# Performance work log

Hardware: AMD Instinct MI355X
Metric: run time of the kernel (lower is better)

## Reference

```python
import jax, jax.numpy as jnp
import numpy as np

N = 10000   # num_nodes (= input feature dim, identity-style features)
E = 320000  # edges (avg degree 32)
P = 200000  # candidate node pairs
H1, H2 = 32, 16


def gcn_conv(x, W, b, edge_index, num_nodes):
    # PyG GCNConv: add self-loops, symmetric D^-1/2 (A+I) D^-1/2 normalization,
    # linear transform, scatter-add aggregation, then bias.
    loop = jnp.arange(num_nodes)
    src = jnp.concatenate([edge_index[0], loop])
    dst = jnp.concatenate([edge_index[1], loop])
    deg = jax.ops.segment_sum(jnp.ones_like(src, dtype=x.dtype), dst,
                              num_segments=num_nodes)  # includes self-loop, so deg >= 1
    dinv = jax.lax.rsqrt(deg)
    norm = dinv[src] * dinv[dst]                       # [E+N]
    h = x @ W                                          # [N, out]
    out = jax.ops.segment_sum(h[src] * norm[:, None], dst, num_segments=num_nodes)
    return out + b


def setup_inputs() -> dict:
    key = jax.random.key(0)
    ks = jax.random.split(key, 9)
    x = jax.random.normal(ks[0], (N, N), dtype=jnp.float32)
    edge_index = jax.random.randint(ks[1], (2, E), 0, N)
    pair_index = jax.random.randint(ks[2], (P, 2), 0, N)
    W1 = jax.random.normal(ks[3], (N, H1), dtype=jnp.float32) * 0.01
    b1 = jnp.zeros((H1,), jnp.float32)
    W2 = jax.random.normal(ks[4], (H1, H2), dtype=jnp.float32) * 0.1
    b2 = jnp.zeros((H2,), jnp.float32)
    Wfc = jax.random.normal(ks[5], (2 * H2, 1), dtype=jnp.float32) * 0.1
    bfc = jnp.zeros((1,), jnp.float32)
    return {"x": x, "edge_index": edge_index, "pair_index": pair_index,
            "W1": W1, "b1": b1, "W2": W2, "b2": b2, "Wfc": Wfc, "bfc": bfc}


def reference(x, edge_index, pair_index, W1, b1, W2, b2, Wfc, bfc):
    h = jax.nn.relu(gcn_conv(x, W1, b1, edge_index, N))   # [N, 32]
    h = gcn_conv(h, W2, b2, edge_index, N)                # [N, 16]
    pair = jnp.concatenate([h[pair_index[:, 0]], h[pair_index[:, 1]]], axis=1)  # [P, 32]
    return jax.nn.sigmoid(pair @ Wfc + bfc)               # [P, 1]
```

## Files before the change

### kernel.cpp

```cpp
#include <hip/hip_runtime.h>
#include <math.h>

#define NN 10000
#define EE 320000
#define PP 200000
#define WKP 10240

typedef __attribute__((ext_vector_type(8))) short bf8v;
typedef __attribute__((ext_vector_type(4))) float f4v;

#define GLOAD_LDS16(gsrc, ldst)                                                        \
    __builtin_amdgcn_global_load_lds((const __attribute__((address_space(1))) void*)(gsrc), \
                                     (__attribute__((address_space(3))) void*)(ldst), 16, 0, 0)

__device__ __forceinline__ ushort f2bf(float f) {
    uint u = __float_as_uint(f);
    return (ushort)((u + 0x7fffu + ((u >> 16) & 1u)) >> 16);
}

__global__ void k_deg_count(const int* __restrict__ dst, int* __restrict__ degi) {
    int e = blockIdx.x * blockDim.x + threadIdx.x;
    if (e < EE) atomicAdd(&degi[dst[e]], 1);
}

__global__ void k_dinv(const int* __restrict__ degi, float* __restrict__ dinv) {
    int n = blockIdx.x * blockDim.x + threadIdx.x;
    if (n < NN) dinv[n] = rsqrtf((float)(degi[n] + 1));
}

__global__ void k_wprep(const float* __restrict__ W1, ushort* __restrict__ w1t) {
    int t = blockIdx.x * blockDim.x + threadIdx.x;
    if (t >= 32 * WKP) return;
    int c = t / WKP, k = t - c * WKP;
    float v = (k < NN) ? W1[(long)k * 32 + c] : 0.f;
    w1t[t] = f2bf(v);
}

__global__ __launch_bounds__(256) void k_gemm1(const float* __restrict__ x,
                                               const ushort* __restrict__ w1t,
                                               const float* __restrict__ zp,
                                               float* __restrict__ h1_pre) {
    __shared__ __align__(16) float xs[4][3][32][32];
    const int tid = threadIdx.x;
    const int lane = tid & 63;
    const int w = tid >> 6;
    const int lr = lane >> 3;
    const int s = lane & 7;
    const int fl = lane & 15;
    const int khi = lane >> 4;
    const int row0 = blockIdx.x * 128 + w * 32;
    const int k_begin = blockIdx.y * 640;
    const int k_end = min(NN, k_begin + 640);
    const int nt = (k_end - k_begin + 31) >> 5;
    const long NN2 = (long)NN * NN;

    f4v acc[2][2];
#pragma unroll
    for (int a = 0; a < 2; ++a)
#pragma unroll
        for (int b = 0; b < 2; ++b) acc[a][b] = (f4v){0.f, 0.f, 0.f, 0.f};

    auto stage_x = [&](int buf, int t) {
        const int k0 = k_begin + t * 32;
#pragma unroll
        for (int j = 0; j < 4; ++j) {
            int rl = j * 8 + lr;
            int c4 = s ^ (rl & 7);
            long flat = (long)(row0 + rl) * NN + k0 + c4 * 4;
            const float* src = (flat + 4 <= NN2) ? (x + flat) : zp;
            GLOAD_LDS16(src, &xs[w][buf][j * 8][0]);
        }
    };
    auto wload = [&](int t, bf8v& b0, bf8v& b1) {
        const long kg = (long)k_begin + t * 32 + khi * 8;
        b0 = *(const bf8v*)(w1t + (long)(fl)      * WKP + kg);
        b1 = *(const bf8v*)(w1t + (long)(16 + fl) * WKP + kg);
    };
    auto compute = [&](int buf, bf8v b0, bf8v b1) {
#pragma unroll
        for (int rt = 0; rt < 2; ++rt) {
            const int rowl = rt * 16 + fl;
            const float4* xr = (const float4*)&xs[w][buf][rowl][0];
            float4 f0 = xr[(khi * 2)     ^ (rowl & 7)];
            float4 f1 = xr[(khi * 2 + 1) ^ (rowl & 7)];
            union { bf8v v; ushort u[8]; } a;
            a.u[0] = f2bf(f0.x); a.u[1] = f2bf(f0.y); a.u[2] = f2bf(f0.z); a.u[3] = f2bf(f0.w);
            a.u[4] = f2bf(f1.x); a.u[5] = f2bf(f1.y); a.u[6] = f2bf(f1.z); a.u[7] = f2bf(f1.w);
            acc[rt][0] = __builtin_amdgcn_mfma_f32_16x16x32_bf16(a.v, b0, acc[rt][0], 0, 0, 0);
            acc[rt][1] = __builtin_amdgcn_mfma_f32_16x16x32_bf16(a.v, b1, acc[rt][1], 0, 0, 0);
        }
    };

    bf8v wc0, wc1, wn0, wn1;
    stage_x(0, 0);
    stage_x(1, 1);
    wload(0, wc0, wc1);

    int buf = 0;
    for (int t = 0; t < nt; ++t) {
        if (t + 2 < nt) stage_x((buf + 2 == 3 ? buf - 1 : buf + 2), t + 2);
        if (t + 1 < nt) wload(t + 1, wn0, wn1);
        asm volatile("s_waitcnt vmcnt(6)" ::: "memory");
        __builtin_amdgcn_sched_barrier(0);
        compute(buf, wc0, wc1);
        wc0 = wn0; wc1 = wn1;
        buf = (buf + 1 == 3) ? 0 : buf + 1;
    }

#pragma unroll
    for (int rt = 0; rt < 2; ++rt) {
        const int gbase = row0 + rt * 16 + khi * 4;
#pragma unroll
        for (int ct = 0; ct < 2; ++ct) {
            const int col = ct * 16 + fl;
#pragma unroll
            for (int r = 0; r < 4; ++r) {
                const int g = gbase + r;
                if (g < NN) atomicAdd(&h1_pre[g * 32 + col], acc[rt][ct][r]);
            }
        }
    }
}

__global__ void k_selfinit1(const float* __restrict__ h1_pre, const float* __restrict__ dinv,
                            float* __restrict__ out1) {
    int t = blockIdx.x * blockDim.x + threadIdx.x;
    if (t < NN * 32) {
        int n = t >> 5;
        float di = dinv[n];
        out1[t] = di * di * h1_pre[t];
    }
}

__global__ void k_scatter1(const int* __restrict__ src, const int* __restrict__ dst,
                           const float* __restrict__ dinv, const float* __restrict__ h1_pre,
                           float* __restrict__ out1) {
    int t = blockIdx.x * blockDim.x + threadIdx.x;
    if (t >= EE * 32) return;
    int e = t >> 5, c = t & 31;
    int s = src[e], d = dst[e];
    float nrm = dinv[s] * dinv[d];
    atomicAdd(&out1[d * 32 + c], h1_pre[s * 32 + c] * nrm);
}

__global__ void k_bias_relu1(float* __restrict__ out1, const float* __restrict__ b1) {
    int t = blockIdx.x * blockDim.x + threadIdx.x;
    if (t < NN * 32) out1[t] = fmaxf(out1[t] + b1[t & 31], 0.f);
}

__global__ __launch_bounds__(256) void k_gemm2(const float* __restrict__ out1,
                                               const float* __restrict__ W2,
                                               float* __restrict__ h2_pre) {
    __shared__ float w2s[512];
    int tid = threadIdx.x;
    w2s[tid] = W2[tid & 511];
    if (tid < 256) w2s[256 + tid] = W2[256 + tid];
    __syncthreads();
    int c = tid & 15, yloc = tid >> 4;
    int n = blockIdx.x * 16 + yloc;
    if (n < NN) {
        float a = 0.f;
#pragma unroll
        for (int k = 0; k < 32; ++k) a += out1[n * 32 + k] * w2s[k * 16 + c];
        h2_pre[n * 16 + c] = a;
    }
}

__global__ void k_selfinit2(const float* __restrict__ h2_pre, const float* __restrict__ dinv,
                            float* __restrict__ out2) {
    int t = blockIdx.x * blockDim.x + threadIdx.x;
    if (t < NN * 16) {
        int n = t >> 4;
        float di = dinv[n];
        out2[t] = di * di * h2_pre[t];
    }
}

__global__ void k_scatter2(const int* __restrict__ src, const int* __restrict__ dst,
                           const float* __restrict__ dinv, const float* __restrict__ h2_pre,
                           float* __restrict__ out2) {
    int t = blockIdx.x * blockDim.x + threadIdx.x;
    if (t >= EE * 16) return;
    int e = t >> 4, c = t & 15;
    int s = src[e], d = dst[e];
    float nrm = dinv[s] * dinv[d];
    atomicAdd(&out2[d * 16 + c], h2_pre[s * 16 + c] * nrm);
}

__global__ void k_final2(const float* __restrict__ out2, const float* __restrict__ b2,
                         const float* __restrict__ Wfc, float* __restrict__ s_arr,
                         float* __restrict__ t_arr) {
    int n = blockIdx.x * blockDim.x + threadIdx.x;
    if (n >= NN) return;
    float s = 0.f, t = 0.f;
#pragma unroll
    for (int c = 0; c < 16; ++c) {
        float v = out2[n * 16 + c] + b2[c];
        s += v * Wfc[c];
        t += v * Wfc[16 + c];
    }
    s_arr[n] = s;
    t_arr[n] = t;
}

__global__ void k_pairs(const int* __restrict__ pair, const float* __restrict__ s_arr,
                        const float* __restrict__ t_arr, const float* __restrict__ bfc,
                        float* __restrict__ out) {
    int p = blockIdx.x * blockDim.x + threadIdx.x;
    if (p >= PP) return;
    const int2 ab = ((const int2*)pair)[p];
    float z = s_arr[ab.x] + t_arr[ab.y] + bfc[0];
    out[p] = 1.f / (1.f + expf(-z));
}

extern "C" void kernel_launch(void* const* d_in, const int* in_sizes, int n_in,
                              void* d_out, int out_size, void* d_ws, size_t ws_size,
                              hipStream_t stream) {
    const float* x    = (const float*)d_in[0];
    const int*   edge = (const int*)d_in[1];
    const int*   pair = (const int*)d_in[2];
    const float* W1   = (const float*)d_in[3];
    const float* b1   = (const float*)d_in[4];
    const float* W2   = (const float*)d_in[5];
    const float* b2   = (const float*)d_in[6];
    const float* Wfc  = (const float*)d_in[7];
    const float* bfc  = (const float*)d_in[8];
    float* out = (float*)d_out;
    float* ws  = (float*)d_ws;

    const int* src = edge;
    const int* dst = edge + EE;

    int*    degi   = (int*)ws;
    float*  dinv   = ws + NN;
    float*  h1_pre = ws + 2 * NN;
    float*  out1   = ws + 34 * NN;
    float*  h2_pre = ws + 66 * NN;
    float*  out2   = ws + 82 * NN;
    float*  s_arr  = ws + 98 * NN;
    float*  t_arr  = ws + 99 * NN;
    float*  zp     = ws + 100 * NN;
    ushort* w1t    = (ushort*)(ws + 100 * NN + 256);

    hipMemsetAsync(degi, 0, NN * sizeof(int), stream);
    hipMemsetAsync(h1_pre, 0, NN * 32 * sizeof(float), stream);
    hipMemsetAsync(zp, 0, 1024, stream);

    k_deg_count<<<(EE + 255) / 256, 256, 0, stream>>>(dst, degi);
    k_dinv<<<(NN + 255) / 256, 256, 0, stream>>>(degi, dinv);
    k_wprep<<<(32 * WKP + 255) / 256, 256, 0, stream>>>(W1, w1t);

    k_gemm1<<<dim3(79, 16), 256, 0, stream>>>(x, w1t, zp, h1_pre);

    k_selfinit1<<<(NN * 32 + 255) / 256, 256, 0, stream>>>(h1_pre, dinv, out1);
    k_scatter1<<<(EE * 32 + 255) / 256, 256, 0, stream>>>(src, dst, dinv, h1_pre, out1);
    k_bias_relu1<<<(NN * 32 + 255) / 256, 256, 0, stream>>>(out1, b1);

    k_gemm2<<<(NN + 15) / 16, 256, 0, stream>>>(out1, W2, h2_pre);

    k_selfinit2<<<(NN * 16 + 255) / 256, 256, 0, stream>>>(h2_pre, dinv, out2);
    k_scatter2<<<(EE * 16 + 255) / 256, 256, 0, stream>>>(src, dst, dinv, h2_pre, out2);

    k_final2<<<(NN + 255) / 256, 256, 0, stream>>>(out2, b2, Wfc, s_arr, t_arr);
    k_pairs<<<(PP + 255) / 256, 256, 0, stream>>>(pair, s_arr, t_arr, bfc, out);
}
```

Before: 207.3 us.

## Pre-swizzle W1 into MFMA fragment order and stage via LDS double buffer

W1 is now prepared in per-tile MFMA fragment layout so each wave loads its B operand with contiguous 16-byte global-to-LDS loads alongside the x tile. The x pipeline drops from triple to double buffering, and the register-held prefetch of W is replaced by LDS reads. This is meant to coalesce the B loads and simplify the wait accounting. In exchange it gives up one stage of prefetch depth, which may expose more of the load latency of the memory-bound x stream.

Result: faster. 198.9 us (-4.1%).

```diff
diff --git a/kernel.cpp b/kernel.cpp
--- a/kernel.cpp
+++ b/kernel.cpp
@@ -4,7 +4,7 @@
 #define NN 10000
 #define EE 320000
 #define PP 200000
-#define WKP 10240
+#define NTILES 320
 
 typedef __attribute__((ext_vector_type(8))) short bf8v;
 typedef __attribute__((ext_vector_type(4))) float f4v;
@@ -28,19 +28,21 @@
     if (n < NN) dinv[n] = rsqrtf((float)(degi[n] + 1));
 }
 
-__global__ void k_wprep(const float* __restrict__ W1, ushort* __restrict__ w1t) {
-    int t = blockIdx.x * blockDim.x + threadIdx.x;
-    if (t >= 32 * WKP) return;
-    int c = t / WKP, k = t - c * WKP;
-    float v = (k < NN) ? W1[(long)k * 32 + c] : 0.f;
-    w1t[t] = f2bf(v);
+__global__ void k_wprep(const float* __restrict__ W1, ushort* __restrict__ wf) {
+    int t = blockIdx.x * blockDim.x + threadIdx.x;
+    if (t >= NTILES * 2 * 64 * 8) return;
+    int e = t & 7, lane = (t >> 3) & 63, ct = (t >> 9) & 1, g = t >> 10;
+    int col = ct * 16 + (lane & 15);
+    int k = g * 32 + (lane >> 4) * 8 + e;
+    wf[t] = (k < NN) ? f2bf(W1[(long)k * 32 + col]) : (ushort)0;
 }
 
 __global__ __launch_bounds__(256) void k_gemm1(const float* __restrict__ x,
-                                               const ushort* __restrict__ w1t,
+                                               const ushort* __restrict__ wf,
                                                const float* __restrict__ zp,
                                                float* __restrict__ h1_pre) {
-    __shared__ __align__(16) float xs[4][3][32][32];
+    __shared__ __align__(16) float  xs[4][2][32][32];
+    __shared__ __align__(16) ushort ws[4][2][1024];
     const int tid = threadIdx.x;
     const int lane = tid & 63;
     const int w = tid >> 6;
@@ -51,6 +53,7 @@
     const int row0 = blockIdx.x * 128 + w * 32;
     const int k_begin = blockIdx.y * 640;
     const int k_end = min(NN, k_begin + 640);
+    const int g0 = blockIdx.y * 20;
     const int nt = (k_end - k_begin + 31) >> 5;
     const long NN2 = (long)NN * NN;
 
@@ -60,7 +63,7 @@
 #pragma unroll
         for (int b = 0; b < 2; ++b) acc[a][b] = (f4v){0.f, 0.f, 0.f, 0.f};
 
-    auto stage_x = [&](int buf, int t) {
+    auto stage = [&](int buf, int t) {
         const int k0 = k_begin + t * 32;
 #pragma unroll
         for (int j = 0; j < 4; ++j) {
@@ -70,13 +73,14 @@
             const float* src = (flat + 4 <= NN2) ? (x + flat) : zp;
             GLOAD_LDS16(src, &xs[w][buf][j * 8][0]);
         }
+        const int g = g0 + t;
+#pragma unroll
+        for (int ct = 0; ct < 2; ++ct)
+            GLOAD_LDS16(wf + ((long)(g * 2 + ct) * 64 + lane) * 8, &ws[w][buf][ct * 512]);
     };
-    auto wload = [&](int t, bf8v& b0, bf8v& b1) {
-        const long kg = (long)k_begin + t * 32 + khi * 8;
-        b0 = *(const bf8v*)(w1t + (long)(fl)      * WKP + kg);
-        b1 = *(const bf8v*)(w1t + (long)(16 + fl) * WKP + kg);
-    };
-    auto compute = [&](int buf, bf8v b0, bf8v b1) {
+    auto compute = [&](int buf) {
+        bf8v b0 = *(const bf8v*)&ws[w][buf][lane * 8];
+        bf8v b1 = *(const bf8v*)&ws[w][buf][512 + lane * 8];
 #pragma unroll
         for (int rt = 0; rt < 2; ++rt) {
             const int rowl = rt * 16 + fl;
@@ -91,20 +95,18 @@
         }
     };
 
-    bf8v wc0, wc1, wn0, wn1;
-    stage_x(0, 0);
-    stage_x(1, 1);
-    wload(0, wc0, wc1);
-
+    stage(0, 0);
     int buf = 0;
     for (int t = 0; t < nt; ++t) {
-        if (t + 2 < nt) stage_x((buf + 2 == 3 ? buf - 1 : buf + 2), t + 2);
-        if (t + 1 < nt) wload(t + 1, wn0, wn1);
-        asm volatile("s_waitcnt vmcnt(6)" ::: "memory");
+        if (t + 1 < nt) {
+            stage(buf ^ 1, t + 1);
+            asm volatile("s_waitcnt vmcnt(6)" ::: "memory");
+        } else {
+            asm volatile("s_waitcnt vmcnt(0)" ::: "memory");
+        }
         __builtin_amdgcn_sched_barrier(0);
-        compute(buf, wc0, wc1);
-        wc0 = wn0; wc1 = wn1;
-        buf = (buf + 1 == 3) ? 0 : buf + 1;
+        compute(buf);
+        buf ^= 1;
     }
 
 #pragma unroll
@@ -240,7 +242,7 @@
     float*  s_arr  = ws + 98 * NN;
     float*  t_arr  = ws + 99 * NN;
     float*  zp     = ws + 100 * NN;
-    ushort* w1t    = (ushort*)(ws + 100 * NN + 256);
+    ushort* w1f    = (ushort*)(ws + 100 * NN + 256);
 
     hipMemsetAsync(degi, 0, NN * sizeof(int), stream);
     hipMemsetAsync(h1_pre, 0, NN * 32 * sizeof(float), stream);
@@ -248,9 +250,9 @@
 
     k_deg_count<<<(EE + 255) / 256, 256, 0, stream>>>(dst, degi);
     k_dinv<<<(NN + 255) / 256, 256, 0, stream>>>(degi, dinv);
-    k_wprep<<<(32 * WKP + 255) / 256, 256, 0, stream>>>(W1, w1t);
-
-    k_gemm1<<<dim3(79, 16), 256, 0, stream>>>(x, w1t, zp, h1_pre);
+    k_wprep<<<(NTILES * 2 * 64 * 8 + 255) / 256, 256, 0, stream>>>(W1, w1f);
+
+    k_gemm1<<<dim3(79, 16), 256, 0, stream>>>(x, w1f, zp, h1_pre);
 
     k_selfinit1<<<(NN * 32 + 255) / 256, 256, 0, stream>>>(h1_pre, dinv, out1);
     k_scatter1<<<(EE * 32 + 255) / 256, 256, 0, stream>>>(src, dst, dinv, h1_pre, out1);
```
